# Optimization experiments

Hardware: AMD Instinct MI355X
Metric: run time of the kernel (lower is better)

The kernel has to match this reference:

```python
import jax, jax.numpy as jnp
import numpy as np

N = 50000   # nodes
E = 800000  # edges
G = 64      # graphs
D_IN = 128
H = 128
H2 = 64  # max(H//2, 8)
H3 = 32  # max(H//4, 8)
OUT = 2
EPS = 1e-5


def setup_inputs() -> dict:
    key = jax.random.key(0)
    ks = jax.random.split(key, 32)

    def w(k, shape, scale=0.05):
        return jax.random.normal(k, shape, dtype=jnp.float32) * scale

    inp = {
        "x": jax.random.normal(ks[0], (N, D_IN), dtype=jnp.float32),
        "edge_src": jax.random.randint(ks[1], (E,), 0, N, dtype=jnp.int32),
        "edge_dst": jax.random.randint(ks[2], (E,), 0, N, dtype=jnp.int32),
        "edge_weight": jax.random.uniform(ks[3], (E,), dtype=jnp.float32),
        "batch": jnp.sort(jax.random.randint(ks[4], (N,), 0, G, dtype=jnp.int32)),
        # GCNConv weights/biases
        "W1": w(ks[5], (D_IN, H)), "b1": jnp.zeros((H,), jnp.float32),
        "W2": w(ks[6], (H, H)),    "b2": jnp.zeros((H,), jnp.float32),
        "W3": w(ks[7], (H, H)),    "b3": jnp.zeros((H,), jnp.float32),
        # BatchNorm affine params
        "g1": jnp.ones((H,), jnp.float32), "be1": jnp.zeros((H,), jnp.float32),
        "g2": jnp.ones((H,), jnp.float32), "be2": jnp.zeros((H,), jnp.float32),
        "g3": jnp.ones((H,), jnp.float32), "be3": jnp.zeros((H,), jnp.float32),
        # MLP head
        "Wm1": w(ks[8], (H, H)),   "bm1": jnp.zeros((H,), jnp.float32),
        "Wm2": w(ks[9], (H, H2)),  "bm2": jnp.zeros((H2,), jnp.float32),
        "Wm3": w(ks[10], (H2, H3)), "bm3": jnp.zeros((H3,), jnp.float32),
        "Wm4": w(ks[11], (H3, OUT)), "bm4": jnp.zeros((OUT,), jnp.float32),
    }
    return inp


def reference(x, edge_src, edge_dst, edge_weight, batch,
              W1, b1, W2, b2, W3, b3,
              g1, be1, g2, be2, g3, be3,
              Wm1, bm1, Wm2, bm2, Wm3, bm3, Wm4, bm4):
    n = x.shape[0]
    loop = jnp.arange(n, dtype=edge_src.dtype)
    # PyG GCNConv default: add self-loops with weight 1, symmetric normalization
    src = jnp.concatenate([edge_src, loop])
    dst = jnp.concatenate([edge_dst, loop])
    w = jnp.concatenate([edge_weight, jnp.ones((n,), x.dtype)])
    deg = jax.ops.segment_sum(w, dst, num_segments=n)              # [N]
    dinv = jnp.where(deg > 0, deg ** -0.5, 0.0)
    norm = dinv[src] * w * dinv[dst]                               # [E+N]

    def gcn_conv(h, W, b):
        h = h @ W                                                  # [N, H]
        msg = norm[:, None] * h[src]                               # gather + scale
        return jax.ops.segment_sum(msg, dst, num_segments=n) + b   # scatter-add

    def bn(h, gamma, beta):
        mu = h.mean(axis=0)
        var = ((h - mu) ** 2).mean(axis=0)   # biased var, as torch BN training
        return (h - mu) * jax.lax.rsqrt(var + EPS) * gamma + beta

    h = jax.nn.relu(bn(gcn_conv(x, W1, b1), g1, be1))
    h = jax.nn.relu(bn(gcn_conv(h, W2, b2), g2, be2))
    h = jax.nn.relu(bn(gcn_conv(h, W3, b3), g3, be3))

    # global mean pool over graphs
    counts = jax.ops.segment_sum(jnp.ones((n,), h.dtype), batch, num_segments=G)
    pooled = jax.ops.segment_sum(h, batch, num_segments=G) / jnp.maximum(counts, 1.0)[:, None]

    # MLP head
    z = jax.nn.relu(pooled @ Wm1 + bm1)
    z = jax.nn.relu(z @ Wm2 + bm2)
    z = jax.nn.relu(z @ Wm3 + bm3)
    return z @ Wm4 + bm4
```

## Files before the change

kernel.cpp:

```cpp
#include <hip/hip_runtime.h>
#include <hip/hip_bf16.h>

#define NN 50000
#define NE 800000
#define NG 64
#define DH 128
#define EPSV 1e-5
#define NBLK_AGG 1000
#define NPB 50
#define SCAN_BLK 256
#define SCAN_NBLK ((NN + SCAN_BLK - 1) / SCAN_BLK)
#define PB_STRIDE 1024


__global__ void edge_count(const int* __restrict__ dst, int* __restrict__ ecnt,
                           int* __restrict__ off) {
    int e = blockIdx.x * 256 + threadIdx.x;
    if (e < NE) off[e] = atomicAdd(&ecnt[dst[e]], 1);
}

__global__ __launch_bounds__(SCAN_BLK) void scan_partial(
    const int* __restrict__ ecnt, int* __restrict__ bsum) {
    int tid = threadIdx.x;
    int i = blockIdx.x * SCAN_BLK + tid;
    int v = (i < NN) ? ecnt[i] : 0;
    __shared__ int sm[SCAN_BLK];
    sm[tid] = v;
    __syncthreads();
    for (int off = SCAN_BLK / 2; off > 0; off >>= 1) {
        if (tid < off) sm[tid] += sm[tid + off];
        __syncthreads();
    }
    if (tid == 0) bsum[blockIdx.x] = sm[0];
}

__global__ __launch_bounds__(SCAN_BLK) void rowptr_write_f(
    const int* __restrict__ ecnt, const int* __restrict__ bsum,
    int* __restrict__ rowptr) {
    __shared__ int sb[256];
    __shared__ int s[SCAN_BLK];
    int tid = threadIdx.x;
    int bv = (tid < SCAN_NBLK) ? bsum[tid] : 0;
    sb[tid] = bv;
    __syncthreads();
    for (int off = 1; off < 256; off <<= 1) {
        int u = (tid >= off) ? sb[tid - off] : 0;
        __syncthreads();
        sb[tid] += u;
        __syncthreads();
    }
    int boff = (blockIdx.x > 0) ? sb[blockIdx.x - 1] : 0;
    int i = blockIdx.x * SCAN_BLK + tid;
    int v = (i < NN) ? ecnt[i] : 0;
    s[tid] = v;
    __syncthreads();
    for (int off = 1; off < SCAN_BLK; off <<= 1) {
        int u = (tid >= off) ? s[tid - off] : 0;
        __syncthreads();
        s[tid] += u;
        __syncthreads();
    }
    if (i < NN) rowptr[i] = s[tid] - v + boff;
    if (i == 0) rowptr[NN] = NE;
}

__global__ void edge_place2(const int* __restrict__ src, const int* __restrict__ dst,
                            const float* __restrict__ w, const int* __restrict__ rowptr,
                            const int* __restrict__ off, int* __restrict__ csr_src,
                            float* __restrict__ csr_w) {
    int e = blockIdx.x * 256 + threadIdx.x;
    if (e < NE) {
        int pos = rowptr[dst[e]] + off[e];
        csr_src[pos] = src[e];
        csr_w[pos] = w[e];
    }
}

__global__ void deg_dinv_csr(const float* __restrict__ csr_w,
                             const int* __restrict__ rowptr,
                             float* __restrict__ dinv) {
    int n = blockIdx.x * 256 + threadIdx.x;
    if (n < NN) {
        float s = 1.0f;
        int e1 = rowptr[n + 1];
        for (int e = rowptr[n]; e < e1; ++e) s += csr_w[e];
        dinv[n] = 1.0f / sqrtf(s);
    }
}


__global__ __launch_bounds__(256) void gemm_fused(
    const float* __restrict__ hin, const float* __restrict__ scale,
    const float* __restrict__ shift, const float* __restrict__ W,
    const float* __restrict__ dinv, __hip_bfloat162* __restrict__ hwb)
{
    __shared__ float Ws[DH * DH];
    __shared__ float hs[32 * DH];
    int tid = threadIdx.x;

    const float4* Wg = (const float4*)W;
    float4* Ws4 = (float4*)Ws;
#pragma unroll
    for (int i = 0; i < 16; ++i) Ws4[tid + i * 256] = Wg[tid + i * 256];

    int row0 = blockIdx.x * 32;
    float4* hs4 = (float4*)hs;
#pragma unroll
    for (int i = 0; i < 4; ++i) {
        int f4 = tid + i * 256;
        int r = f4 >> 5;
        int c4 = f4 & 31;
        int row = row0 + r;
        float4 v = make_float4(0.f, 0.f, 0.f, 0.f);
        if (row < NN) {
            v = ((const float4*)hin)[row * 32 + c4];
            if (scale) {
                int c = c4 * 4;
                v.x = fmaxf(v.x * scale[c + 0] + shift[c + 0], 0.f);
                v.y = fmaxf(v.y * scale[c + 1] + shift[c + 1], 0.f);
                v.z = fmaxf(v.z * scale[c + 2] + shift[c + 2], 0.f);
                v.w = fmaxf(v.w * scale[c + 3] + shift[c + 3], 0.f);
            }
        }
        hs4[f4] = v;
    }
    __syncthreads();

    int ct = tid & 31;
    int rg = tid >> 5;
    float4 acc0 = make_float4(0, 0, 0, 0), acc1 = acc0, acc2 = acc0, acc3 = acc0;

#pragma unroll 8
    for (int k = 0; k < DH; ++k) {
        float4 wv = Ws4[k * 32 + ct];
        float a0 = hs[(rg * 4 + 0) * DH + k];
        float a1 = hs[(rg * 4 + 1) * DH + k];
        float a2 = hs[(rg * 4 + 2) * DH + k];
        float a3 = hs[(rg * 4 + 3) * DH + k];
        acc0.x += a0 * wv.x; acc0.y += a0 * wv.y; acc0.z += a0 * wv.z; acc0.w += a0 * wv.w;
        acc1.x += a1 * wv.x; acc1.y += a1 * wv.y; acc1.z += a1 * wv.z; acc1.w += a1 * wv.w;
        acc2.x += a2 * wv.x; acc2.y += a2 * wv.y; acc2.z += a2 * wv.z; acc2.w += a2 * wv.w;
        acc3.x += a3 * wv.x; acc3.y += a3 * wv.y; acc3.z += a3 * wv.z; acc3.w += a3 * wv.w;
    }

    float4 accs[4] = {acc0, acc1, acc2, acc3};
#pragma unroll
    for (int j = 0; j < 4; ++j) {
        int row = row0 + rg * 4 + j;
        if (row < NN) {
            float di = dinv[row];
            hwb[row * 64 + ct * 2 + 0] =
                __float22bfloat162_rn(make_float2(accs[j].x * di, accs[j].y * di));
            hwb[row * 64 + ct * 2 + 1] =
                __float22bfloat162_rn(make_float2(accs[j].z * di, accs[j].w * di));
        }
    }
}


__global__ __launch_bounds__(512) void agg_csr(
    const __hip_bfloat162* __restrict__ hwb, const int* __restrict__ rowptr,
    const int* __restrict__ csr_src, const float* __restrict__ csr_w,
    const float* __restrict__ b, const float* __restrict__ dinv,
    float2* __restrict__ agg2, double* __restrict__ pblock_t)
{
    int tid = threadIdx.x;
    int lane = tid & 63;
    int w = tid >> 6;
    float2 bb = ((const float2*)b)[lane];
    double sx = 0.0, sy = 0.0, qx = 0.0, qy = 0.0;
    int n0 = blockIdx.x * NPB;
    int n1 = min(n0 + NPB, NN);
    for (int node = n0 + w; node < n1; node += 8) {
        float di = dinv[node];
        float2 h = __bfloat1622float2(hwb[node * 64 + lane]);
        float accx = h.x;
        float accy = h.y;
        int e = rowptr[node], e1 = rowptr[node + 1];
        for (; e + 8 <= e1; e += 8) {
            int a0 = csr_src[e + 0];
            int a1 = csr_src[e + 1];
            int a2 = csr_src[e + 2];
            int a3 = csr_src[e + 3];
            int a4 = csr_src[e + 4];
            int a5 = csr_src[e + 5];
            int a6 = csr_src[e + 6];
            int a7 = csr_src[e + 7];
            float w0 = csr_w[e + 0];
            float w1 = csr_w[e + 1];
            float w2 = csr_w[e + 2];
            float w3 = csr_w[e + 3];
            float w4 = csr_w[e + 4];
            float w5 = csr_w[e + 5];
            float w6 = csr_w[e + 6];
            float w7 = csr_w[e + 7];
            float2 v0 = __bfloat1622float2(hwb[a0 * 64 + lane]);
            float2 v1 = __bfloat1622float2(hwb[a1 * 64 + lane]);
            float2 v2 = __bfloat1622float2(hwb[a2 * 64 + lane]);
            float2 v3 = __bfloat1622float2(hwb[a3 * 64 + lane]);
            float2 v4 = __bfloat1622float2(hwb[a4 * 64 + lane]);
            float2 v5 = __bfloat1622float2(hwb[a5 * 64 + lane]);
            float2 v6 = __bfloat1622float2(hwb[a6 * 64 + lane]);
            float2 v7 = __bfloat1622float2(hwb[a7 * 64 + lane]);
            accx += w0 * v0.x; accy += w0 * v0.y;
            accx += w1 * v1.x; accy += w1 * v1.y;
            accx += w2 * v2.x; accy += w2 * v2.y;
            accx += w3 * v3.x; accy += w3 * v3.y;
            accx += w4 * v4.x; accy += w4 * v4.y;
            accx += w5 * v5.x; accy += w5 * v5.y;
            accx += w6 * v6.x; accy += w6 * v6.y;
            accx += w7 * v7.x; accy += w7 * v7.y;
        }
        for (; e + 4 <= e1; e += 4) {
            int a0 = csr_src[e + 0];
            int a1 = csr_src[e + 1];
            int a2 = csr_src[e + 2];
            int a3 = csr_src[e + 3];
            float w0 = csr_w[e + 0];
            float w1 = csr_w[e + 1];
            float w2 = csr_w[e + 2];
            float w3 = csr_w[e + 3];
            float2 v0 = __bfloat1622float2(hwb[a0 * 64 + lane]);
            float2 v1 = __bfloat1622float2(hwb[a1 * 64 + lane]);
            float2 v2 = __bfloat1622float2(hwb[a2 * 64 + lane]);
            float2 v3 = __bfloat1622float2(hwb[a3 * 64 + lane]);
            accx += w0 * v0.x; accy += w0 * v0.y;
            accx += w1 * v1.x; accy += w1 * v1.y;
            accx += w2 * v2.x; accy += w2 * v2.y;
            accx += w3 * v3.x; accy += w3 * v3.y;
        }
        for (; e < e1; ++e) {
            float wn = csr_w[e];
            float2 v = __bfloat1622float2(hwb[csr_src[e] * 64 + lane]);
            accx += wn * v.x; accy += wn * v.y;
        }
        float ox = accx * di + bb.x;
        float oy = accy * di + bb.y;
        agg2[node * 64 + lane] = make_float2(ox, oy);
        sx += (double)ox; qx += (double)ox * (double)ox;
        sy += (double)oy; qy += (double)oy * (double)oy;
    }
    __shared__ double shx[8][64], shy[8][64], qhx[8][64], qhy[8][64];
    shx[w][lane] = sx; shy[w][lane] = sy;
    qhx[w][lane] = qx; qhy[w][lane] = qy;
    __syncthreads();
    if (tid < 128) {
        int d = tid;
        int ls = d >> 1;
        int comp = d & 1;
        double ssum = 0.0, qsum = 0.0;
#pragma unroll
        for (int ww = 0; ww < 8; ++ww) {
            ssum += comp ? shy[ww][ls] : shx[ww][ls];
            qsum += comp ? qhy[ww][ls] : qhx[ww][ls];
        }
        pblock_t[d * PB_STRIDE + blockIdx.x]         = ssum;
        pblock_t[(128 + d) * PB_STRIDE + blockIdx.x] = qsum;
    }
}

__global__ __launch_bounds__(256) void bn_reduce_t(
    const double* __restrict__ pblock_t, const float* __restrict__ g,
    const float* __restrict__ be, float* __restrict__ scale,
    float* __restrict__ shift)
{
    int d = blockIdx.x;
    int tid = threadIdx.x;
    double s = 0.0, q = 0.0;
    for (int i = tid; i < NBLK_AGG; i += 256) {
        s += pblock_t[d * PB_STRIDE + i];
        q += pblock_t[(128 + d) * PB_STRIDE + i];
    }
    __shared__ double ss[256], qq[256];
    ss[tid] = s; qq[tid] = q;
    __syncthreads();
    for (int off = 128; off > 0; off >>= 1) {
        if (tid < off) { ss[tid] += ss[tid + off]; qq[tid] += qq[tid + off]; }
        __syncthreads();
    }
    if (tid == 0) {
        double mu = ss[0] / (double)NN;
        double ex2 = qq[0] / (double)NN;
        double var = ex2 - mu * mu;
        double sc = (double)g[d] / sqrt(var + (double)EPSV);
        scale[d] = (float)sc;
        shift[d] = (float)((double)be[d] - mu * sc);
    }
}


__global__ __launch_bounds__(256) void pool_mlp(
    const float* __restrict__ agg, const float* __restrict__ scale,
    const float* __restrict__ shift, const int* __restrict__ batch,
    const float* __restrict__ Wm1, const float* __restrict__ bm1,
    const float* __restrict__ Wm2, const float* __restrict__ bm2,
    const float* __restrict__ Wm3, const float* __restrict__ bm3,
    const float* __restrict__ Wm4, const float* __restrict__ bm4,
    float* __restrict__ out)
{
    int g = blockIdx.x;
    int tid = threadIdx.x;
    auto lb = [&](int key) {
        int lo = 0, hi = NN;
        while (lo < hi) { int mid = (lo + hi) >> 1; if (batch[mid] < key) lo = mid + 1; else hi = mid; }
        return lo;
    };
    int lo = lb(g), hi = lb(g + 1);

    int d = tid & 127;
    int half = tid >> 7;
    float sc = scale[d], sh = shift[d];
    double acc = 0.0;
    for (int r = lo + half; r < hi; r += 2)
        acc += (double)fmaxf(agg[r * DH + d] * sc + sh, 0.f);

    __shared__ double pm[256];
    __shared__ float za[DH], zb[DH];
    pm[tid] = acc;
    __syncthreads();
    if (tid < 128) {
        double cf = (double)((hi - lo) > 0 ? (hi - lo) : 1);
        za[tid] = (float)((pm[tid] + pm[tid + 128]) / cf);
    }
    __syncthreads();
    float a;
    if (tid < 128) {
        a = bm1[tid];
        for (int k = 0; k < 128; ++k) a += za[k] * Wm1[k * 128 + tid];
        zb[tid] = fmaxf(a, 0.f);
    }
    __syncthreads();
    if (tid < 64) {
        a = bm2[tid];
        for (int k = 0; k < 128; ++k) a += zb[k] * Wm2[k * 64 + tid];
        za[tid] = fmaxf(a, 0.f);
    }
    __syncthreads();
    if (tid < 32) {
        a = bm3[tid];
        for (int k = 0; k < 64; ++k) a += za[k] * Wm3[k * 32 + tid];
        zb[tid] = fmaxf(a, 0.f);
    }
    __syncthreads();
    if (tid < 2) {
        a = bm4[tid];
        for (int k = 0; k < 32; ++k) a += zb[k] * Wm4[k * 2 + tid];
        out[g * 2 + tid] = a;
    }
}


extern "C" void kernel_launch(void* const* d_in, const int* in_sizes, int n_in,
                              void* d_out, int out_size, void* d_ws, size_t ws_size,
                              hipStream_t stream) {
    const float* x  = (const float*)d_in[0];
    const int* esrc = (const int*)d_in[1];
    const int* edst = (const int*)d_in[2];
    const float* ew = (const float*)d_in[3];
    const int* batch = (const int*)d_in[4];
    const float* W1 = (const float*)d_in[5];  const float* b1 = (const float*)d_in[6];
    const float* W2 = (const float*)d_in[7];  const float* b2 = (const float*)d_in[8];
    const float* W3 = (const float*)d_in[9];  const float* b3 = (const float*)d_in[10];
    const float* g1 = (const float*)d_in[11]; const float* be1 = (const float*)d_in[12];
    const float* g2 = (const float*)d_in[13]; const float* be2 = (const float*)d_in[14];
    const float* g3 = (const float*)d_in[15]; const float* be3 = (const float*)d_in[16];
    const float* Wm1 = (const float*)d_in[17]; const float* bm1 = (const float*)d_in[18];
    const float* Wm2 = (const float*)d_in[19]; const float* bm2 = (const float*)d_in[20];
    const float* Wm3 = (const float*)d_in[21]; const float* bm3 = (const float*)d_in[22];
    const float* Wm4 = (const float*)d_in[23]; const float* bm4 = (const float*)d_in[24];
    float* out = (float*)d_out;

    char* ws = (char*)d_ws;
    int*    ecnt   = (int*)(ws + 0);
    float*  dinv   = (float*)(ws + 200192);
    float*  scale0 = (float*)(ws + 400384);
    int*    bsum   = (int*)(ws + 403456);
    int*    rowptr = (int*)(ws + 404480);
    int*    csr_src = (int*)(ws + 604672);
    float*  csr_w   = (float*)(ws + 3804672);
    double* pblock_t = (double*)(ws + 7004672);
    __hip_bfloat162* hwb = (__hip_bfloat162*)(ws + 9101824);
    float*  aggA   = (float*)(ws + 21901824);
    float*  aggB   = (float*)(ws + 47501824);
    int*    off    = (int*)(ws + 47501824);

    hipMemsetAsync(d_ws, 0, 200192, stream);

    edge_count<<<(NE + 255) / 256, 256, 0, stream>>>(edst, ecnt, off);
    scan_partial<<<SCAN_NBLK, SCAN_BLK, 0, stream>>>(ecnt, bsum);
    rowptr_write_f<<<SCAN_NBLK, SCAN_BLK, 0, stream>>>(ecnt, bsum, rowptr);
    edge_place2<<<(NE + 255) / 256, 256, 0, stream>>>(esrc, edst, ew, rowptr, off,
                                                      csr_src, csr_w);
    deg_dinv_csr<<<(NN + 255) / 256, 256, 0, stream>>>(csr_w, rowptr, dinv);

    const float* Ws_[3] = {W1, W2, W3};
    const float* bs_[3] = {b1, b2, b3};
    const float* gs_[3] = {g1, g2, g3};
    const float* bes_[3] = {be1, be2, be3};
    float* aggs[3] = {aggA, aggB, aggA};
    const int gemm_grid = (NN + 31) / 32;

    const float* curIn = x;
    const float* curScale = nullptr;
    const float* curShift = nullptr;
    for (int l = 0; l < 3; ++l) {
        float* agg = aggs[l];
        gemm_fused<<<gemm_grid, 256, 0, stream>>>(curIn, curScale, curShift,
                                                  Ws_[l], dinv, hwb);
        agg_csr<<<NBLK_AGG, 512, 0, stream>>>(hwb, rowptr, csr_src,
                                              csr_w, bs_[l], dinv,
                                              (float2*)agg, pblock_t);
        float* sc = scale0 + l * 256;
        float* sh = sc + 128;
        bn_reduce_t<<<128, 256, 0, stream>>>(pblock_t, gs_[l], bes_[l], sc, sh);
        curIn = agg;
        curScale = sc;
        curShift = sh;
    }

    pool_mlp<<<NG, 256, 0, stream>>>(aggA, curScale, curShift, batch,
                                     Wm1, bm1, Wm2, bm2, Wm3, bm3, Wm4, bm4, out);
}
```

Before: 525.6 us.

## Split pooling into row-chunked atomic reduction kernel and separate MLP kernel

The old pool_mlp kernel used only 64 blocks, each streaming all rows of one graph (about 780 rows × 128 floats). Pooling now runs in 500 blocks over fixed row chunks, accumulating runs of equal batch id and flushing them to a zeroed double buffer with atomics. A separate 64-block kernel then divides by the node counts and runs the MLP head. The goal is to spread the final reduction across the whole GPU, at the cost of one extra launch, fp64 atomics and a larger memset.

```diff
diff --git a/kernel.cpp b/kernel.cpp
--- a/kernel.cpp
+++ b/kernel.cpp
@@ -289,9 +289,37 @@
 }
 
 
-__global__ __launch_bounds__(256) void pool_mlp(
+#define POOL_CHUNK 100
+__global__ __launch_bounds__(256) void pool_k(
     const float* __restrict__ agg, const float* __restrict__ scale,
     const float* __restrict__ shift, const int* __restrict__ batch,
+    double* __restrict__ pooled)
+{
+    int tid = threadIdx.x;
+    int d = tid & 127;
+    int rl = tid >> 7;
+    float sc = scale[d], sh = shift[d];
+    int r0 = blockIdx.x * POOL_CHUNK;
+    int rend = r0 + POOL_CHUNK;
+    if (rend > NN) rend = NN;
+    double acc = 0.0;
+    int gc = -1;
+    for (int r = r0 + rl; r < rend; r += 2) {
+        int g = batch[r];
+        float v = agg[r * DH + d];
+        v = fmaxf(v * sc + sh, 0.f);
+        if (g != gc) {
+            if (gc >= 0) unsafeAtomicAdd(&pooled[gc * DH + d], acc);
+            gc = g; acc = 0.0;
+        }
+        acc += (double)v;
+    }
+    if (gc >= 0) unsafeAtomicAdd(&pooled[gc * DH + d], acc);
+}
+
+
+__global__ __launch_bounds__(128) void mlp_k(
+    const double* __restrict__ pooled, const int* __restrict__ batch,
     const float* __restrict__ Wm1, const float* __restrict__ bm1,
     const float* __restrict__ Wm2, const float* __restrict__ bm2,
     const float* __restrict__ Wm3, const float* __restrict__ bm3,
@@ -305,47 +333,31 @@
         while (lo < hi) { int mid = (lo + hi) >> 1; if (batch[mid] < key) lo = mid + 1; else hi = mid; }
         return lo;
     };
-    int lo = lb(g), hi = lb(g + 1);
-
-    int d = tid & 127;
-    int half = tid >> 7;
-    float sc = scale[d], sh = shift[d];
-    double acc = 0.0;
-    for (int r = lo + half; r < hi; r += 2)
-        acc += (double)fmaxf(agg[r * DH + d] * sc + sh, 0.f);
-
-    __shared__ double pm[256];
+    int cntg = lb(g + 1) - lb(g);
     __shared__ float za[DH], zb[DH];
-    pm[tid] = acc;
-    __syncthreads();
-    if (tid < 128) {
-        double cf = (double)((hi - lo) > 0 ? (hi - lo) : 1);
-        za[tid] = (float)((pm[tid] + pm[tid + 128]) / cf);
-    }
-    __syncthreads();
-    float a;
-    if (tid < 128) {
-        a = bm1[tid];
-        for (int k = 0; k < 128; ++k) a += za[k] * Wm1[k * 128 + tid];
-        zb[tid] = fmaxf(a, 0.f);
-    }
+    float cf = fmaxf((float)cntg, 1.0f);
+    za[tid] = (float)(pooled[g * DH + tid] / (double)cf);
+    __syncthreads();
+    float acc = bm1[tid];
+    for (int k = 0; k < 128; ++k) acc += za[k] * Wm1[k * 128 + tid];
+    zb[tid] = fmaxf(acc, 0.f);
     __syncthreads();
     if (tid < 64) {
-        a = bm2[tid];
-        for (int k = 0; k < 128; ++k) a += zb[k] * Wm2[k * 64 + tid];
-        za[tid] = fmaxf(a, 0.f);
+        acc = bm2[tid];
+        for (int k = 0; k < 128; ++k) acc += zb[k] * Wm2[k * 64 + tid];
+        za[tid] = fmaxf(acc, 0.f);
     }
     __syncthreads();
     if (tid < 32) {
-        a = bm3[tid];
-        for (int k = 0; k < 64; ++k) a += za[k] * Wm3[k * 32 + tid];
-        zb[tid] = fmaxf(a, 0.f);
+        acc = bm3[tid];
+        for (int k = 0; k < 64; ++k) acc += za[k] * Wm3[k * 32 + tid];
+        zb[tid] = fmaxf(acc, 0.f);
     }
     __syncthreads();
     if (tid < 2) {
-        a = bm4[tid];
-        for (int k = 0; k < 32; ++k) a += zb[k] * Wm4[k * 2 + tid];
-        out[g * 2 + tid] = a;
+        acc = bm4[tid];
+        for (int k = 0; k < 32; ++k) acc += zb[k] * Wm4[k * 2 + tid];
+        out[g * 2 + tid] = acc;
     }
 }
 
@@ -372,19 +384,20 @@
 
     char* ws = (char*)d_ws;
     int*    ecnt   = (int*)(ws + 0);
-    float*  dinv   = (float*)(ws + 200192);
-    float*  scale0 = (float*)(ws + 400384);
-    int*    bsum   = (int*)(ws + 403456);
-    int*    rowptr = (int*)(ws + 404480);
-    int*    csr_src = (int*)(ws + 604672);
-    float*  csr_w   = (float*)(ws + 3804672);
-    double* pblock_t = (double*)(ws + 7004672);
-    __hip_bfloat162* hwb = (__hip_bfloat162*)(ws + 9101824);
-    float*  aggA   = (float*)(ws + 21901824);
-    float*  aggB   = (float*)(ws + 47501824);
-    int*    off    = (int*)(ws + 47501824);
-
-    hipMemsetAsync(d_ws, 0, 200192, stream);
+    double* pooled = (double*)(ws + 200192);
+    float*  dinv   = (float*)(ws + 265728);
+    float*  scale0 = (float*)(ws + 465984);
+    int*    bsum   = (int*)(ws + 469056);
+    int*    rowptr = (int*)(ws + 471104);
+    int*    csr_src = (int*)(ws + 671744);
+    float*  csr_w   = (float*)(ws + 3871744);
+    double* pblock_t = (double*)(ws + 7071744);
+    __hip_bfloat162* hwb = (__hip_bfloat162*)(ws + 9323648);
+    float*  aggA   = (float*)(ws + 22123648);
+    float*  aggB   = (float*)(ws + 47723648);
+    int*    off    = (int*)(ws + 47723648);
+
+    hipMemsetAsync(d_ws, 0, 265728, stream);
 
     edge_count<<<(NE + 255) / 256, 256, 0, stream>>>(edst, ecnt, off);
     scan_partial<<<SCAN_NBLK, SCAN_BLK, 0, stream>>>(ecnt, bsum);
@@ -418,6 +431,8 @@
         curShift = sh;
     }
 
-    pool_mlp<<<NG, 256, 0, stream>>>(aggA, curScale, curShift, batch,
-                                     Wm1, bm1, Wm2, bm2, Wm3, bm3, Wm4, bm4, out);
-}
+    pool_k<<<(NN + POOL_CHUNK - 1) / POOL_CHUNK, 256, 0, stream>>>(
+        aggA, curScale, curShift, batch, pooled);
+    mlp_k<<<NG, 128, 0, stream>>>(pooled, batch, Wm1, bm1, Wm2, bm2, Wm3, bm3,
+                                  Wm4, bm4, out);
+}
```

Result: faster. 427.9 us (-18.6%).
